# Performance work log

Measured on AMD Instinct MI355X. Metric: run time of the kernel, lower is better.

Reference implementation:

```python
import jax, jax.numpy as jnp
import numpy as np

N_NODES = 100000
C = 128
E = 800000
V = 50000
NEG_SLOPE = 0.2


def gat_conv(x, edges, W, att_src, att_dst, bias, num_nodes):
    """Single-head PyG-style GATConv with self-loops added (PyG default).

    edges: [2, E] with row 0 = source j, row 1 = destination i.
    """
    loops = jnp.arange(num_nodes, dtype=edges.dtype)
    src = jnp.concatenate([edges[0], loops])  # [E+N]
    dst = jnp.concatenate([edges[1], loops])

    h = x @ W.T                               # [N, C] linear transform
    a_s = h @ att_src                         # [N] per-node src score
    a_d = h @ att_dst                         # [N] per-node dst score

    e = jax.nn.leaky_relu(a_s[src] + a_d[dst], NEG_SLOPE)  # [E+N]
    # scatter-softmax over edges grouped by destination node
    m = jax.ops.segment_max(e, dst, num_segments=num_nodes)
    ex = jnp.exp(e - m[dst])
    denom = jax.ops.segment_sum(ex, dst, num_segments=num_nodes)
    alpha = ex / (denom[dst] + 1e-16)         # [E+N]

    out = jax.ops.segment_sum(alpha[:, None] * h[src], dst, num_segments=num_nodes)
    return out + bias


def setup_inputs() -> dict:
    key = jax.random.key(0)
    ks = jax.random.split(key, 12)
    s = 1.0 / np.sqrt(C)
    return {
        "embedding": jax.random.normal(ks[0], (N_NODES, C), jnp.float32),
        "W1": jax.random.normal(ks[1], (C, C), jnp.float32) * s,
        "att_src1": jax.random.normal(ks[2], (C,), jnp.float32) * s,
        "att_dst1": jax.random.normal(ks[3], (C,), jnp.float32) * s,
        "b1": jax.random.normal(ks[4], (C,), jnp.float32) * s,
        "W2": jax.random.normal(ks[5], (C, C), jnp.float32) * s,
        "att_src2": jax.random.normal(ks[6], (C,), jnp.float32) * s,
        "att_dst2": jax.random.normal(ks[7], (C,), jnp.float32) * s,
        "b2": jax.random.normal(ks[8], (C,), jnp.float32) * s,
        "edges1": jax.random.randint(ks[9], (2, E), 0, N_NODES, jnp.int64 if jax.config.jax_enable_x64 else jnp.int32),
        "edges2": jax.random.randint(ks[10], (2, E), 0, N_NODES, jnp.int64 if jax.config.jax_enable_x64 else jnp.int32),
        "idx_mapping": jax.random.randint(ks[11], (V,), 0, N_NODES, jnp.int64 if jax.config.jax_enable_x64 else jnp.int32),
    }


def reference(embedding, W1, att_src1, att_dst1, b1, W2, att_src2, att_dst2, b2,
              edges1, edges2, idx_mapping):
    h = gat_conv(embedding, edges1, W1, att_src1, att_dst1, b1, N_NODES)
    h = gat_conv(h, edges2, W2, att_src2, att_dst2, b2, N_NODES)
    return h[idx_mapping]
```

## Files before the change

kernel.cpp:

```cpp
#include <hip/hip_runtime.h>

#define N_NODES 100000
#define C_DIM 128
#define E_EDGES 800000
#define V_OUT 50000
#define EN (E_EDGES + N_NODES)
#define M2 (2 * N_NODES)
#define EN2 (2 * EN)

#define BSHIFT 9
#define NBUCK_L ((N_NODES + 511) >> 9)
#define NBUCK2 (2 * NBUCK_L)
#define CAP 8192
#define P1_CHUNK 4096
#define P1_PER_T (P1_CHUNK / 256)
#define NCHUNK ((EN2 + P1_CHUNK - 1) / P1_CHUNK)
#define VFLAG_BLKS ((V_OUT + 255) / 256)

#define XPAD 136
#define LDS_E 768

#define NCHUNKS_G ((N_NODES + 63) / 64)
#define GEMM_GRID 512

typedef unsigned int uint;
typedef unsigned short ushort;
typedef __attribute__((ext_vector_type(8))) short bf16x8;
typedef __attribute__((ext_vector_type(4))) float f32x4;

static __device__ __forceinline__ ushort f2bf(float f) {
    uint u = __float_as_uint(f);
    u += 0x7fffu + ((u >> 16) & 1);
    return (ushort)(u >> 16);
}

template <int IN_F32>
__global__ __launch_bounds__(256) void gemm_mfma(
    const void* __restrict__ xin, const float* __restrict__ W,
    const float* __restrict__ att_s, const float* __restrict__ att_d,
    ushort* __restrict__ hb, float* __restrict__ a_s, float* __restrict__ a_d)
{
    __shared__ ushort ws[128 * XPAD];
    __shared__ ushort xs[2][64 * XPAD];
    const int tid = threadIdx.x;

    {
        const int row = tid >> 1, half = tid & 1;
        const float* src = W + row * 128 + half * 64;
        ushort* dst = &ws[row * XPAD + half * 64];
        #pragma unroll
        for (int i = 0; i < 8; ++i) {
            float4 u = *reinterpret_cast<const float4*>(src + i * 8);
            float4 v = *reinterpret_cast<const float4*>(src + i * 8 + 4);
            uint4 pk;
            pk.x = (uint)f2bf(u.x) | ((uint)f2bf(u.y) << 16);
            pk.y = (uint)f2bf(u.z) | ((uint)f2bf(u.w) << 16);
            pk.z = (uint)f2bf(v.x) | ((uint)f2bf(v.y) << 16);
            pk.w = (uint)f2bf(v.z) | ((uint)f2bf(v.w) << 16);
            *reinterpret_cast<uint4*>(dst + i * 8) = pk;
        }
    }

    const int srow_t = tid >> 2, q = tid & 3;
    const int lane = tid & 63, wv = tid >> 6;
    const int m = lane & 15, quad = lane >> 4;

    int c = blockIdx.x;
    float4 pf_f[8];
    uint4  pf_b[4];

    {
        const long srow = min((long)c * 64 + srow_t, (long)N_NODES - 1);
        if (IN_F32) {
            const float* src = (const float*)xin + srow * 128 + q * 32;
            #pragma unroll
            for (int i = 0; i < 8; ++i)
                pf_f[i] = *reinterpret_cast<const float4*>(src + i * 4);
        } else {
            const ushort* src = (const ushort*)xin + srow * 128 + q * 32;
            #pragma unroll
            for (int i = 0; i < 4; ++i)
                pf_b[i] = *reinterpret_cast<const uint4*>(src + i * 8);
        }
        ushort* dst = &xs[0][srow_t * XPAD + q * 32];
        if (IN_F32) {
            #pragma unroll
            for (int i = 0; i < 4; ++i) {
                uint4 pk;
                pk.x = (uint)f2bf(pf_f[2*i].x)   | ((uint)f2bf(pf_f[2*i].y)   << 16);
                pk.y = (uint)f2bf(pf_f[2*i].z)   | ((uint)f2bf(pf_f[2*i].w)   << 16);
                pk.z = (uint)f2bf(pf_f[2*i+1].x) | ((uint)f2bf(pf_f[2*i+1].y) << 16);
                pk.w = (uint)f2bf(pf_f[2*i+1].z) | ((uint)f2bf(pf_f[2*i+1].w) << 16);
                *reinterpret_cast<uint4*>(dst + i * 8) = pk;
            }
        } else {
            #pragma unroll
            for (int i = 0; i < 4; ++i)
                *reinterpret_cast<uint4*>(dst + i * 8) = pf_b[i];
        }
    }
    __syncthreads();

    int cur = 0;
    while (c < NCHUNKS_G) {
        const int cn = c + GEMM_GRID;

        if (cn < NCHUNKS_G) {
            const long srow = min((long)cn * 64 + srow_t, (long)N_NODES - 1);
            if (IN_F32) {
                const float* src = (const float*)xin + srow * 128 + q * 32;
                #pragma unroll
                for (int i = 0; i < 8; ++i)
                    pf_f[i] = *reinterpret_cast<const float4*>(src + i * 4);
            } else {
                const ushort* src = (const ushort*)xin + srow * 128 + q * 32;
                #pragma unroll
                for (int i = 0; i < 4; ++i)
                    pf_b[i] = *reinterpret_cast<const uint4*>(src + i * 8);
            }
        }

        const int n0 = c * 64 + wv * 16;
        bf16x8 a[4];
        #pragma unroll
        for (int ki = 0; ki < 4; ++ki)
            a[ki] = *reinterpret_cast<const bf16x8*>(&xs[cur][(wv*16+m)*XPAD + quad*8 + ki*32]);
        __syncthreads();

        float ps[4] = {0, 0, 0, 0}, pd[4] = {0, 0, 0, 0};
        #pragma unroll
        for (int ct = 0; ct < 8; ++ct) {
            const int cc = ct * 16 + m;
            f32x4 acc = {0.f, 0.f, 0.f, 0.f};
            #pragma unroll
            for (int ki = 0; ki < 4; ++ki) {
                bf16x8 b = *reinterpret_cast<const bf16x8*>(&ws[cc*XPAD + quad*8 + ki*32]);
                acc = __builtin_amdgcn_mfma_f32_16x16x32_bf16(a[ki], b, acc, 0, 0, 0);
            }
            const float asc = att_s[cc], adc = att_d[cc];
            #pragma unroll
            for (int r = 0; r < 4; ++r) {
                xs[cur][(wv*16 + quad*4 + r) * XPAD + cc] = f2bf(acc[r]);
                ps[r] = fmaf(acc[r], asc, ps[r]);
                pd[r] = fmaf(acc[r], adc, pd[r]);
            }
        }
        __syncthreads();

        {
            const int sub = tid & 15, rb = tid >> 4;
            #pragma unroll
            for (int i = 0; i < 4; ++i) {
                const int rl = rb + i * 16;
                const int node = c * 64 + rl;
                uint4 v = *reinterpret_cast<const uint4*>(&xs[cur][rl * XPAD + sub * 8]);
                if (node < N_NODES)
                    *reinterpret_cast<uint4*>(hb + (long)node * 128 + sub * 8) = v;
            }
        }
        #pragma unroll
        for (int r = 0; r < 4; ++r) {
            float s = ps[r], d = pd[r];
            #pragma unroll
            for (int x = 1; x < 16; x <<= 1) { s += __shfl_xor(s, x); d += __shfl_xor(d, x); }
            const int node = n0 + quad * 4 + r;
            if (m == 0 && node < N_NODES) { a_s[node] = s; a_d[node] = d; }
        }

        if (cn < NCHUNKS_G) {
            ushort* dst = &xs[cur ^ 1][srow_t * XPAD + q * 32];
            if (IN_F32) {
                #pragma unroll
                for (int i = 0; i < 4; ++i) {
                    uint4 pk;
                    pk.x = (uint)f2bf(pf_f[2*i].x)   | ((uint)f2bf(pf_f[2*i].y)   << 16);
                    pk.y = (uint)f2bf(pf_f[2*i].z)   | ((uint)f2bf(pf_f[2*i].w)   << 16);
                    pk.z = (uint)f2bf(pf_f[2*i+1].x) | ((uint)f2bf(pf_f[2*i+1].y) << 16);
                    pk.w = (uint)f2bf(pf_f[2*i+1].z) | ((uint)f2bf(pf_f[2*i+1].w) << 16);
                    *reinterpret_cast<uint4*>(dst + i * 8) = pk;
                }
            } else {
                #pragma unroll
                for (int i = 0; i < 4; ++i)
                    *reinterpret_cast<uint4*>(dst + i * 8) = pf_b[i];
            }
        }
        __syncthreads();
        cur ^= 1;
        c = cn;
    }
}

__global__ __launch_bounds__(256) void partition_kernel(
    const int* __restrict__ e1, const int* __restrict__ e2,
    int* __restrict__ cursor, uint* __restrict__ slab,
    const int* __restrict__ idxm, int* __restrict__ vflag)
{
    __shared__ int cnt[NBUCK2];
    __shared__ int basearr[NBUCK2];
    const int tid = threadIdx.x;
    const int blk = blockIdx.x;
    if (blk >= NCHUNK) {
        int v = (blk - NCHUNK) * 256 + tid;
        if (v < V_OUT) vflag[idxm[v]] = 1;
        return;
    }
    for (int i = tid; i < NBUCK2; i += 256) cnt[i] = 0;
    __syncthreads();

    const int e0 = blk * P1_CHUNK;
    uint ent[P1_PER_T];
    int  bkt[P1_PER_T];
    #pragma unroll
    for (int i = 0; i < P1_PER_T; ++i) {
        int e = e0 + i * 256 + tid;
        bkt[i] = -1;
        if (e < EN2) {
            int src, dst, lb;
            if (e < EN) {
                if (e < E_EDGES) { src = e1[e]; dst = e1[E_EDGES + e]; }
                else             { src = dst = e - E_EDGES; }
                lb = 0;
            } else {
                int f = e - EN;
                if (f < E_EDGES) { src = e2[f]; dst = e2[E_EDGES + f]; }
                else             { src = dst = f - E_EDGES; }
                lb = NBUCK_L;
            }
            bkt[i] = lb + (dst >> BSHIFT);
            ent[i] = (uint)src | ((uint)(dst & 511) << 17);
            atomicAdd(&cnt[bkt[i]], 1);
        }
    }
    __syncthreads();
    for (int b = tid; b < NBUCK2; b += 256) {
        int c = cnt[b];
        basearr[b] = (c > 0) ? atomicAdd(&cursor[b], c) : 0;
        cnt[b] = 0;
    }
    __syncthreads();
    #pragma unroll
    for (int i = 0; i < P1_PER_T; ++i) {
        if (bkt[i] >= 0) {
            int r = basearr[bkt[i]] + atomicAdd(&cnt[bkt[i]], 1);
            if (r < CAP) slab[(long)bkt[i] * CAP + r] = ent[i];
        }
    }
}

__global__ __launch_bounds__(256) void local_csr(
    const uint* __restrict__ slab, const int* __restrict__ cursor,
    int* __restrict__ offs, uint* __restrict__ esrc)
{
    __shared__ uint ent[CAP];
    __shared__ int deg[512];
    __shared__ int excl[512];
    __shared__ int sbase;
    const int b = blockIdx.x;
    const int tid = threadIdx.x;
    const int cnt = min(cursor[b], CAP);
    const int layer = (b >= NBUCK_L);
    const int node0 = (b - layer * NBUCK_L) << BSHIFT;
    const int obase = layer * N_NODES;
    const int nodes_n = min(512, N_NODES - node0);

    for (int i = tid; i < 512; i += 256) deg[i] = 0;
    if (tid < 64) {
        int s = 0;
        #pragma unroll
        for (int k = 0; k < 7; ++k) {
            int idx = tid + 64 * k;
            if (idx < b) s += cursor[idx];
        }
        #pragma unroll
        for (int d = 32; d > 0; d >>= 1) s += __shfl_down(s, d);
        if (tid == 0) sbase = s;
    }
    __syncthreads();
    const int base = sbase;

    for (int i = tid; i < cnt; i += 256) {
        uint v = slab[(long)b * CAP + i];
        ent[i] = v;
        atomicAdd(&deg[v >> 17], 1);
    }
    __syncthreads();
    if (tid < 64) {
        int v8[8]; int s = 0;
        #pragma unroll
        for (int i = 0; i < 8; ++i) { v8[i] = deg[tid * 8 + i]; s += v8[i]; }
        int incl = s;
        #pragma unroll
        for (int d = 1; d < 64; d <<= 1) {
            int t = __shfl_up(incl, d);
            if (tid >= d) incl += t;
        }
        int e = incl - s;
        #pragma unroll
        for (int i = 0; i < 8; ++i) { excl[tid * 8 + i] = e; e += v8[i]; }
    }
    __syncthreads();
    for (int i = tid; i < nodes_n; i += 256)
        offs[obase + node0 + i] = base + excl[i];
    for (int i = tid; i < 512; i += 256) deg[i] = 0;
    if (tid == 0 && node0 + 512 >= N_NODES)
        offs[obase + N_NODES] = base + cnt;
    __syncthreads();
    for (int i = tid; i < cnt; i += 256) {
        uint v = ent[i];
        int dl = v >> 17;
        int r = atomicAdd(&deg[dl], 1);
        esrc[base + excl[dl] + r] = v;
    }
}

template <int MODE>
__global__ __launch_bounds__(256) void aggregate(
    const ushort* __restrict__ hb, const float* __restrict__ a_s,
    const float* __restrict__ a_d, const float* __restrict__ bias,
    const int* __restrict__ offs, const uint* __restrict__ esrc,
    const int* __restrict__ vflag, void* __restrict__ outp, int obase)
{
    __shared__ uint2 ew[LDS_E];
    const int tid = threadIdx.x;
    const int node0 = blockIdx.x * 16;
    const int bnode0 = (node0 >> BSHIFT) << BSHIFT;
    const int bstart = offs[obase + node0];
    const int bend   = offs[obase + node0 + 16];
    const int nE = bend - bstart;

    for (int i = tid; i < min(nE, LDS_E); i += 256) {
        uint v = esrc[bstart + i];
        float w = 0.0f;
        const int d = bnode0 + (v >> 17);
        if (MODE == 0 || vflag[d] != 0) {
            float e = a_s[v & 0x1ffff] + a_d[d];
            e = (e >= 0.0f) ? e : 0.2f * e;
            w = __expf(e);
        }
        ew[i] = make_uint2(v, __float_as_uint(w));
    }
    __syncthreads();

    const int wave = tid >> 6;
    const int lane = tid & 63;
    const int slot = lane >> 4;
    const int c16  = lane & 15;
    const int node = node0 + wave * 4 + slot;
    if (MODE == 1 && vflag[node] == 0) return;

    const int start = offs[obase + node];
    const int end   = offs[obase + node + 1];
    const long coff = (long)(c16 << 3);
    float acc[8] = {0, 0, 0, 0, 0, 0, 0, 0};
    float dsum = 0.0f;

    if (start < end) {
        if (nE <= LDS_E) {
            const int jr = start - bstart, jend = end - bstart;
            const int e1 = jend - 1;
            uint2 p0 = ew[jr];
            uint2 p1 = ew[min(jr + 1, e1)];
            uint2 p2 = ew[min(jr + 2, e1)];
            uint2 p3 = ew[min(jr + 3, e1)];
            uint4 h0 = *reinterpret_cast<const uint4*>(hb + ((long)(p0.x & 0x1ffff) << 7) + coff);
            uint4 h1 = *reinterpret_cast<const uint4*>(hb + ((long)(p1.x & 0x1ffff) << 7) + coff);
            uint4 h2 = *reinterpret_cast<const uint4*>(hb + ((long)(p2.x & 0x1ffff) << 7) + coff);
            uint4 h3 = *reinterpret_cast<const uint4*>(hb + ((long)(p3.x & 0x1ffff) << 7) + coff);
            float w0 = __uint_as_float(p0.y);
            float w1 = __uint_as_float(p1.y);
            float w2 = __uint_as_float(p2.y);
            float w3 = __uint_as_float(p3.y);
            for (int j = jr; j < jend; ++j) {
                uint2 p4 = ew[min(j + 4, e1)];
                uint4 h4 = *reinterpret_cast<const uint4*>(hb + ((long)(p4.x & 0x1ffff) << 7) + coff);
                float w4 = __uint_as_float(p4.y);
                dsum += w0;
                acc[0] = fmaf(w0, __uint_as_float(h0.x << 16),         acc[0]);
                acc[1] = fmaf(w0, __uint_as_float(h0.x & 0xffff0000u), acc[1]);
                acc[2] = fmaf(w0, __uint_as_float(h0.y << 16),         acc[2]);
                acc[3] = fmaf(w0, __uint_as_float(h0.y & 0xffff0000u), acc[3]);
                acc[4] = fmaf(w0, __uint_as_float(h0.z << 16),         acc[4]);
                acc[5] = fmaf(w0, __uint_as_float(h0.z & 0xffff0000u), acc[5]);
                acc[6] = fmaf(w0, __uint_as_float(h0.w << 16),         acc[6]);
                acc[7] = fmaf(w0, __uint_as_float(h0.w & 0xffff0000u), acc[7]);
                w0 = w1; w1 = w2; w2 = w3; w3 = w4;
                h0 = h1; h1 = h2; h2 = h3; h3 = h4;
            }
        } else {
            const float ad = a_d[node];
            for (int j = start; j < end; ++j) {
                uint v = esrc[j];
                float e = a_s[v & 0x1ffff] + ad;
                e = (e >= 0.0f) ? e : 0.2f * e;
                float w = __expf(e);
                uint4 h = *reinterpret_cast<const uint4*>(hb + ((long)(v & 0x1ffff) << 7) + coff);
                dsum += w;
                acc[0] = fmaf(w, __uint_as_float(h.x << 16),         acc[0]);
                acc[1] = fmaf(w, __uint_as_float(h.x & 0xffff0000u), acc[1]);
                acc[2] = fmaf(w, __uint_as_float(h.y << 16),         acc[2]);
                acc[3] = fmaf(w, __uint_as_float(h.y & 0xffff0000u), acc[3]);
                acc[4] = fmaf(w, __uint_as_float(h.z << 16),         acc[4]);
                acc[5] = fmaf(w, __uint_as_float(h.z & 0xffff0000u), acc[5]);
                acc[6] = fmaf(w, __uint_as_float(h.w << 16),         acc[6]);
                acc[7] = fmaf(w, __uint_as_float(h.w & 0xffff0000u), acc[7]);
            }
        }
    }

    const float inv = 1.0f / (dsum + 1e-16f);
    const int c0 = c16 << 3;
    const float4 b0 = *reinterpret_cast<const float4*>(bias + c0);
    const float4 b1 = *reinterpret_cast<const float4*>(bias + c0 + 4);
    float res[8];
    res[0] = fmaf(acc[0], inv, b0.x);
    res[1] = fmaf(acc[1], inv, b0.y);
    res[2] = fmaf(acc[2], inv, b0.z);
    res[3] = fmaf(acc[3], inv, b0.w);
    res[4] = fmaf(acc[4], inv, b1.x);
    res[5] = fmaf(acc[5], inv, b1.y);
    res[6] = fmaf(acc[6], inv, b1.z);
    res[7] = fmaf(acc[7], inv, b1.w);
    if (MODE == 0) {
        uint4 pk;
        pk.x = (uint)f2bf(res[0]) | ((uint)f2bf(res[1]) << 16);
        pk.y = (uint)f2bf(res[2]) | ((uint)f2bf(res[3]) << 16);
        pk.z = (uint)f2bf(res[4]) | ((uint)f2bf(res[5]) << 16);
        pk.w = (uint)f2bf(res[6]) | ((uint)f2bf(res[7]) << 16);
        *reinterpret_cast<uint4*>((ushort*)outp + ((long)node << 7) + c0) = pk;
    } else {
        float* op = (float*)outp + ((long)node << 7) + c0;
        *reinterpret_cast<float4*>(op)     = make_float4(res[0], res[1], res[2], res[3]);
        *reinterpret_cast<float4*>(op + 4) = make_float4(res[4], res[5], res[6], res[7]);
    }
}

__global__ void gather_out(const float* __restrict__ h, const int* __restrict__ idx,
                           float* __restrict__ out)
{
    int g = blockIdx.x * 256 + threadIdx.x;
    int v = g >> 5, c4 = (g & 31) << 2;
    long src = (long)idx[v] * C_DIM + c4;
    *reinterpret_cast<float4*>(out + ((long)v * C_DIM + c4)) =
        *reinterpret_cast<const float4*>(h + src);
}

extern "C" void kernel_launch(void* const* d_in, const int* in_sizes, int n_in,
                              void* d_out, int out_size, void* d_ws, size_t ws_size,
                              hipStream_t stream)
{
    const float* emb = (const float*)d_in[0];
    const float* W1  = (const float*)d_in[1];
    const float* as1 = (const float*)d_in[2];
    const float* ad1 = (const float*)d_in[3];
    const float* b1  = (const float*)d_in[4];
    const float* W2  = (const float*)d_in[5];
    const float* as2 = (const float*)d_in[6];
    const float* ad2 = (const float*)d_in[7];
    const float* b2  = (const float*)d_in[8];
    const int* edges1 = (const int*)d_in[9];
    const int* edges2 = (const int*)d_in[10];
    const int* idxm   = (const int*)d_in[11];
    float* out = (float*)d_out;

    char* p = (char*)d_ws;
    auto alloc = [&](size_t bytes) {
        char* r = p;
        p += (bytes + 255) & ~(size_t)255;
        return r;
    };
    float*  hB   = (float*)alloc((size_t)N_NODES * C_DIM * 4);
    ushort* hb   = (ushort*)alloc((size_t)N_NODES * C_DIM * 2);
    ushort* a1o  = (ushort*)alloc((size_t)N_NODES * C_DIM * 2);
    uint*   slab = (uint*)alloc((size_t)NBUCK2 * CAP * 4);
    uint*   esrc = (uint*)alloc((size_t)EN2 * 4);
    int*    offs = (int*)alloc((size_t)(M2 + 1) * 4);
    float*  aS   = (float*)alloc((size_t)N_NODES * 4);
    float*  aD   = (float*)alloc((size_t)N_NODES * 4);
    int*  cursor = (int*)alloc((size_t)NBUCK2 * 4);
    int*  vflag  = (int*)alloc((size_t)N_NODES * 4);

    hipMemsetAsync(cursor, 0, (size_t)((char*)vflag - (char*)cursor) + (size_t)N_NODES * 4, stream);

    partition_kernel<<<NCHUNK + VFLAG_BLKS, 256, 0, stream>>>(
        edges1, edges2, cursor, slab, idxm, vflag);
    local_csr<<<NBUCK2, 256, 0, stream>>>(slab, cursor, offs, esrc);

    gemm_mfma<1><<<GEMM_GRID, 256, 0, stream>>>(emb, W1, as1, ad1, hb, aS, aD);
    aggregate<0><<<N_NODES / 16, 256, 0, stream>>>(hb, aS, aD, b1, offs, esrc, vflag, a1o, 0);

    gemm_mfma<0><<<GEMM_GRID, 256, 0, stream>>>(a1o, W2, as2, ad2, hb, aS, aD);
    aggregate<1><<<N_NODES / 16, 256, 0, stream>>>(hb, aS, aD, b2, offs, esrc, vflag, hB, N_NODES);

    gather_out<<<(V_OUT * 32) / 256, 256, 0, stream>>>(hB, idxm, out);
}
```

Baseline: 275.1 us.

## Fuse final gather into layer-2 aggregation via per-node output linked lists

Replaces the vflag bitmap with a per-node head/next linked list of output rows built atomically from idx_mapping during partitioning. The second aggregation then writes each needed node's result straight to every output row that maps to it. This removes the fp32 intermediate buffer, the gather_out kernel launch and its extra read/write traffic. It adds a second memset and serial list walks for duplicated indices.

```diff
diff --git a/kernel.cpp b/kernel.cpp
--- a/kernel.cpp
+++ b/kernel.cpp
@@ -194,7 +194,7 @@
 __global__ __launch_bounds__(256) void partition_kernel(
     const int* __restrict__ e1, const int* __restrict__ e2,
     int* __restrict__ cursor, uint* __restrict__ slab,
-    const int* __restrict__ idxm, int* __restrict__ vflag)
+    const int* __restrict__ idxm, int* __restrict__ head, int* __restrict__ nextp)
 {
     __shared__ int cnt[NBUCK2];
     __shared__ int basearr[NBUCK2];
@@ -202,7 +202,11 @@
     const int blk = blockIdx.x;
     if (blk >= NCHUNK) {
         int v = (blk - NCHUNK) * 256 + tid;
-        if (v < V_OUT) vflag[idxm[v]] = 1;
+        if (v < V_OUT) {
+            int n = idxm[v];
+            int old = atomicExch(&head[n], v);
+            nextp[v] = old;
+        }
         return;
     }
     for (int i = tid; i < NBUCK2; i += 256) cnt[i] = 0;
@@ -319,7 +323,8 @@
     const ushort* __restrict__ hb, const float* __restrict__ a_s,
     const float* __restrict__ a_d, const float* __restrict__ bias,
     const int* __restrict__ offs, const uint* __restrict__ esrc,
-    const int* __restrict__ vflag, void* __restrict__ outp, int obase)
+    const int* __restrict__ head, const int* __restrict__ nextp,
+    void* __restrict__ outp, int obase)
 {
     __shared__ uint2 ew[LDS_E];
     const int tid = threadIdx.x;
@@ -333,7 +338,7 @@
         uint v = esrc[bstart + i];
         float w = 0.0f;
         const int d = bnode0 + (v >> 17);
-        if (MODE == 0 || vflag[d] != 0) {
+        if (MODE == 0 || head[d] >= 0) {
             float e = a_s[v & 0x1ffff] + a_d[d];
             e = (e >= 0.0f) ? e : 0.2f * e;
             w = __expf(e);
@@ -347,7 +352,11 @@
     const int slot = lane >> 4;
     const int c16  = lane & 15;
     const int node = node0 + wave * 4 + slot;
-    if (MODE == 1 && vflag[node] == 0) return;
+    int hv = 0;
+    if (MODE == 1) {
+        hv = head[node];
+        if (hv < 0) return;
+    }
 
     const int start = offs[obase + node];
     const int end   = offs[obase + node + 1];
@@ -429,20 +438,14 @@
         pk.w = (uint)f2bf(res[6]) | ((uint)f2bf(res[7]) << 16);
         *reinterpret_cast<uint4*>((ushort*)outp + ((long)node << 7) + c0) = pk;
     } else {
-        float* op = (float*)outp + ((long)node << 7) + c0;
-        *reinterpret_cast<float4*>(op)     = make_float4(res[0], res[1], res[2], res[3]);
-        *reinterpret_cast<float4*>(op + 4) = make_float4(res[4], res[5], res[6], res[7]);
-    }
-}
-
-__global__ void gather_out(const float* __restrict__ h, const int* __restrict__ idx,
-                           float* __restrict__ out)
-{
-    int g = blockIdx.x * 256 + threadIdx.x;
-    int v = g >> 5, c4 = (g & 31) << 2;
-    long src = (long)idx[v] * C_DIM + c4;
-    *reinterpret_cast<float4*>(out + ((long)v * C_DIM + c4)) =
-        *reinterpret_cast<const float4*>(h + src);
+        const float4 r0 = make_float4(res[0], res[1], res[2], res[3]);
+        const float4 r1 = make_float4(res[4], res[5], res[6], res[7]);
+        for (int v = hv; v >= 0; v = nextp[v]) {
+            float* op = (float*)outp + ((long)v << 7) + c0;
+            *reinterpret_cast<float4*>(op)     = r0;
+            *reinterpret_cast<float4*>(op + 4) = r1;
+        }
+    }
 }
 
 extern "C" void kernel_launch(void* const* d_in, const int* in_sizes, int n_in,
@@ -469,7 +472,6 @@
         p += (bytes + 255) & ~(size_t)255;
         return r;
     };
-    float*  hB   = (float*)alloc((size_t)N_NODES * C_DIM * 4);
     ushort* hb   = (ushort*)alloc((size_t)N_NODES * C_DIM * 2);
     ushort* a1o  = (ushort*)alloc((size_t)N_NODES * C_DIM * 2);
     uint*   slab = (uint*)alloc((size_t)NBUCK2 * CAP * 4);
@@ -478,19 +480,19 @@
     float*  aS   = (float*)alloc((size_t)N_NODES * 4);
     float*  aD   = (float*)alloc((size_t)N_NODES * 4);
     int*  cursor = (int*)alloc((size_t)NBUCK2 * 4);
-    int*  vflag  = (int*)alloc((size_t)N_NODES * 4);
-
-    hipMemsetAsync(cursor, 0, (size_t)((char*)vflag - (char*)cursor) + (size_t)N_NODES * 4, stream);
+    int*  head   = (int*)alloc((size_t)N_NODES * 4);
+    int*  nextp  = (int*)alloc((size_t)V_OUT * 4);
+
+    hipMemsetAsync(cursor, 0, (size_t)NBUCK2 * 4, stream);
+    hipMemsetAsync(head, 0xFF, (size_t)N_NODES * 4, stream);
 
     partition_kernel<<<NCHUNK + VFLAG_BLKS, 256, 0, stream>>>(
-        edges1, edges2, cursor, slab, idxm, vflag);
+        edges1, edges2, cursor, slab, idxm, head, nextp);
     local_csr<<<NBUCK2, 256, 0, stream>>>(slab, cursor, offs, esrc);
 
     gemm_mfma<1><<<GEMM_GRID, 256, 0, stream>>>(emb, W1, as1, ad1, hb, aS, aD);
-    aggregate<0><<<N_NODES / 16, 256, 0, stream>>>(hb, aS, aD, b1, offs, esrc, vflag, a1o, 0);
+    aggregate<0><<<N_NODES / 16, 256, 0, stream>>>(hb, aS, aD, b1, offs, esrc, head, nextp, a1o, 0);
 
     gemm_mfma<0><<<GEMM_GRID, 256, 0, stream>>>(a1o, W2, as2, ad2, hb, aS, aD);
-    aggregate<1><<<N_NODES / 16, 256, 0, stream>>>(hb, aS, aD, b2, offs, esrc, vflag, hB, N_NODES);
-
-    gather_out<<<(V_OUT * 32) / 256, 256, 0, stream>>>(hB, idxm, out);
-}
+    aggregate<1><<<N_NODES / 16, 256, 0, stream>>>(hb, aS, aD, b2, offs, esrc, head, nextp, out, N_NODES);
+}
```

Result: faster. 266.9 us (-3.0%).
